# Kernel optimization log

Measured on AMD Instinct MI355X. Metric: run time of the kernel, lower is better.

Reference implementation:

```python
import jax, jax.numpy as jnp
import numpy as np

KDIM = 256
KNN = 32
VALUE_EXPAND = 4
EPS = 1e-5


def _ln_last(x, w):
    # LayerNorm over last axis with affine weight w (no bias)
    m = jnp.mean(x, axis=-1, keepdims=True)
    v = jnp.var(x, axis=-1, keepdims=True)
    return (x - m) * jax.lax.rsqrt(v + EPS) * w


def setup_inputs() -> dict:
    key = jax.random.key(0)
    ks = jax.random.split(key, 10)
    B, S, H = 2, 2048, 2048
    head, rank, mh = 2, 2, 2
    key_num = 1024
    value_num = 262144
    vvn = VALUE_EXPAND * value_num  # 1048576
    vdim = 256
    return {
        "hidden_state": jax.random.normal(ks[0], (B, S, H), jnp.float32),
        "wq": jax.random.normal(ks[1], (H, 2 * KDIM), jnp.float32) / np.sqrt(KDIM),
        "qnorm_w": jnp.full((KDIM,), 1.0 / KDIM ** 0.33, jnp.float32),
        "knorm_w": jnp.full((KDIM,), 1.0 / KDIM ** 0.33, jnp.float32),
        "keys": jax.random.normal(ks[2], (head, 2, key_num, KDIM, rank), jnp.float32) / np.sqrt(KDIM),
        "tucker_core": jax.random.uniform(ks[3], (mh, head, rank, rank), jnp.float32),
        "tucker_u": jax.random.normal(ks[4], (1, head, 1, rank), jnp.float32),
        "tucker_v": jax.random.normal(ks[5], (1, head, 1, rank), jnp.float32),
        "values": jax.random.normal(ks[6], (value_num, vdim), jnp.float32) * 0.02,
        "wv": jax.random.normal(ks[7], (VALUE_EXPAND * vdim, H), jnp.float32) / np.sqrt(VALUE_EXPAND * vdim),
        "shuffle_index": jax.random.permutation(ks[8], vvn).astype(jnp.int32),
    }


def reference(hidden_state, wq, qnorm_w, knorm_w, keys, tucker_core,
              tucker_u, tucker_v, values, wv, shuffle_index):
    B, S, H = hidden_state.shape
    bs = B * S
    head, _, key_num, kdim, rank = keys.shape
    value_num, vdim = values.shape

    # query projection + per-half layernorm
    q = (hidden_state.reshape(bs, H) @ wq).reshape(bs, 2, kdim)
    q = _ln_last(q, qnorm_w)
    q1, q2 = q[:, 0], q[:, 1]  # (bs, kdim)

    # keys layernorm over kdim (axis=-2)
    km = jnp.mean(keys, axis=-2, keepdims=True)
    kv = jnp.var(keys, axis=-2, keepdims=True)
    keysn = (keys - km) * jax.lax.rsqrt(kv + EPS) * knorm_w[:, None]

    # per-head, per-rank inner products (all heads share the single query; nhead_share_query=2)
    s1r = jnp.einsum("bd,hkdr->bhkr", q1, keysn[:, 0])  # (bs, head, key_num, rank)
    s2r = jnp.einsum("bd,hkdr->bhkr", q2, keysn[:, 1])

    # rank-1 tucker fused scores + topk along keys
    s1 = (s1r * tucker_u).sum(-1)  # (bs, head, key_num)
    s2 = (s2r * tucker_v).sum(-1)
    _, i1 = jax.lax.top_k(s1, KNN)  # (bs, head, knn)
    _, i2 = jax.lax.top_k(s2, KNN)

    g1 = jnp.take_along_axis(s1r, i1[..., None], axis=2)  # (bs, head, knn, rank)
    g2 = jnp.take_along_axis(s2r, i2[..., None], axis=2)

    # full tucker scores on the knn x knn candidate grid, summed over tucker heads
    all_scores = jnp.einsum("bhkr,mhrs,bhls->bhkl", g1, tucker_core, g2).reshape(bs, head, KNN * KNN)
    all_indices = (i1[..., :, None] * key_num + i2[..., None, :]).reshape(bs, head, KNN * KNN)

    best_scores, bi = jax.lax.top_k(all_scores, KNN)  # (bs, head, knn)
    best_indice = jnp.take_along_axis(all_indices, bi, axis=-1)

    # implicit value expansion: shuffled virtual index -> (expand slot, real value)
    shuffled = shuffle_index[best_indice]
    vidx = shuffled % value_num
    eidx = shuffled // value_num  # in [0, VALUE_EXPAND)
    vals = values[vidx]  # (bs, head, knn, vdim)
    w = jax.nn.softmax(best_scores, axis=-1)
    oh = jax.nn.one_hot(eidx, VALUE_EXPAND, dtype=vals.dtype)  # (bs, head, knn, E)
    agg = jnp.einsum("bhke,bhkv->bev", oh, w[..., None] * vals).reshape(bs, VALUE_EXPAND * vdim)
    out = agg @ wv  # (bs, H)
    return out.reshape(B, S, H)
```

## Files before the change

### kernel.cpp

```cpp
#include <hip/hip_runtime.h>
#include <float.h>
#include <math.h>


typedef __attribute__((ext_vector_type(8))) __bf16 bf16x8;
typedef __attribute__((ext_vector_type(4))) float f32x4;

__device__ __forceinline__ unsigned short f2bf(float x) {
  unsigned int u = __float_as_uint(x);
  return (unsigned short)((u + 0x7FFFu + ((u >> 16) & 1u)) >> 16);
}

__device__ __forceinline__ float wave_sum(float x) {
#pragma unroll
  for (int o = 32; o; o >>= 1) x += __shfl_xor(x, o, 64);
  return x;
}

__device__ __forceinline__ void gll16(const float* g, float* l) {
  __builtin_amdgcn_global_load_lds(
      (const __attribute__((address_space(1))) void*)g,
      (__attribute__((address_space(3))) void*)l, 16, 0, 0);
}

__device__ __forceinline__ unsigned int f2key(float f) {
  const unsigned int u = __float_as_uint(f);
  return u ^ (((unsigned int)((int)u >> 31)) | 0x80000000u);
}
__device__ __forceinline__ float key2f(unsigned int k) {
  return __uint_as_float((k & 0x80000000u) ? (k ^ 0x80000000u) : ~k);
}

__global__ void k_prep32(const float* __restrict__ keys, const float* __restrict__ knw,
                         const float* __restrict__ tu, const float* __restrict__ tv,
                         unsigned short* __restrict__ Bctbf, float* __restrict__ Bg) {
  const int bid = blockIdx.x;
  const int lane = threadIdx.x;
  const int k = bid & 1023, h = (bid >> 10) & 1, c = bid >> 11;
  const float* base = keys + (size_t)((h * 2 + c) * 1024 + k) * 512;
  float x0[4], x1[4];
  float s0 = 0.f, s1 = 0.f, sq0 = 0.f, sq1 = 0.f;
#pragma unroll
  for (int i = 0; i < 4; ++i) {
    const int d = lane + i * 64;
    const float2 p = *(const float2*)&base[d * 2];
    x0[i] = p.x; x1[i] = p.y;
    s0 += p.x; sq0 += p.x * p.x;
    s1 += p.y; sq1 += p.y * p.y;
  }
  s0 = wave_sum(s0); sq0 = wave_sum(sq0);
  s1 = wave_sum(s1); sq1 = wave_sum(sq1);
  const float m0 = s0 * (1.f / 256.f), m1 = s1 * (1.f / 256.f);
  const float rs0 = 1.f / sqrtf(sq0 * (1.f / 256.f) - m0 * m0 + 1e-5f);
  const float rs1 = 1.f / sqrtf(sq1 * (1.f / 256.f) - m1 * m1 + 1e-5f);
  const float* uv = c ? tv : tu;
  const float u0 = uv[h * 2 + 0], u1 = uv[h * 2 + 1];
  const int chk = c * 2048 + h * 1024 + k;
  float* bg = Bg + (size_t)chk * 512;
  unsigned short* bc = Bctbf + (size_t)chk * 256;
#pragma unroll
  for (int i = 0; i < 4; ++i) {
    const int d = lane + i * 64;
    const float w = knw[d];
    const float y0 = (x0[i] - m0) * rs0 * w;
    const float y1 = (x1[i] - m1) * rs1 * w;
    bg[d] = y0;
    bg[256 + d] = y1;
    bc[d] = f2bf(y0 * u0 + y1 * u1);
  }
}

__global__ __launch_bounds__(256) void k_tr32(const float* __restrict__ src,
                                              float* __restrict__ dst, int R, int C) {
  __shared__ float t[64][65];
  const int br = blockIdx.x * 64, bc = blockIdx.y * 64;
  const int tid = threadIdx.x;
  for (int idx = tid; idx < 4096; idx += 256) {
    const int r = idx >> 6, c = idx & 63;
    t[r][c] = src[(size_t)(br + r) * C + bc + c];
  }
  __syncthreads();
  for (int idx = tid; idx < 4096; idx += 256) {
    const int cc = idx >> 6, rr = idx & 63;
    dst[(size_t)(bc + cc) * R + br + rr] = t[rr][cc];
  }
}

template <int SPLITK>
__global__ __launch_bounds__(256) void k_gemm32(
    const float* __restrict__ AT, int lda,
    const float* __restrict__ BT, int ldb, int bsk, int m_split,
    float* __restrict__ C, int M, int N, int K) {
  constexpr int BK = 16;
  __shared__ float As[2][BK][128];
  __shared__ float Bs[2][BK][128];
  const int tid = threadIdx.x;
  const int lane = tid & 63;
  const int w = tid >> 6;
  const int tx = tid & 15, ty = tid >> 4;
  const int bm = blockIdx.x * 128, bn = blockIdx.y * 128;
  const int bcol = bn + ((bm >= m_split) ? bsk : 0);
  const int Ks = K / SPLITK;
  const int kbeg = blockIdx.z * Ks;
  float* Cp = C + (size_t)blockIdx.z * M * N;
  const int l5 = lane >> 5, l31 = lane & 31;
  float acc[8][8] = {};

  auto stage = [&](int buf, int t) {
    const int k0 = t * BK;
#pragma unroll
    for (int i = 0; i < 2; ++i) {
      const int rr = w * 4 + i * 2;
      const size_t krow = (size_t)(kbeg + k0 + rr + l5);
      gll16(&AT[krow * lda + bm + l31 * 4], &As[buf][rr][0]);
      gll16(&BT[krow * ldb + bcol + l31 * 4], &Bs[buf][rr][0]);
    }
  };

  const int T = Ks / BK;
  stage(0, 0);
  __syncthreads();
  int cur = 0;
  for (int t = 0; t < T; ++t) {
    if (t + 1 < T) stage(cur ^ 1, t + 1);
#pragma unroll
    for (int kk = 0; kk < BK; ++kk) {
      float a[8], b[8];
      *(float4*)&a[0] = *(const float4*)&As[cur][kk][ty * 4];
      *(float4*)&a[4] = *(const float4*)&As[cur][kk][64 + ty * 4];
      *(float4*)&b[0] = *(const float4*)&Bs[cur][kk][tx * 4];
      *(float4*)&b[4] = *(const float4*)&Bs[cur][kk][64 + tx * 4];
#pragma unroll
      for (int i = 0; i < 8; ++i)
#pragma unroll
        for (int j = 0; j < 8; ++j) acc[i][j] += a[i] * b[j];
    }
    __syncthreads();
    cur ^= 1;
  }
#pragma unroll
  for (int ih = 0; ih < 2; ++ih)
#pragma unroll
    for (int i = 0; i < 4; ++i) {
      const size_t r = bm + ih * 64 + ty * 4 + i;
#pragma unroll
      for (int jh = 0; jh < 2; ++jh) {
        float4 v = {acc[ih * 4 + i][jh * 4 + 0], acc[ih * 4 + i][jh * 4 + 1],
                    acc[ih * 4 + i][jh * 4 + 2], acc[ih * 4 + i][jh * 4 + 3]};
        *(float4*)&Cp[r * N + bn + jh * 64 + tx * 4] = v;
      }
    }
}

__global__ void k_ln_q(const float* __restrict__ qpart, const float* __restrict__ qnw,
                       float* __restrict__ q12n, unsigned short* __restrict__ q12bf) {
  const int bid = blockIdx.x;
  const int lane = threadIdx.x;
  const int b = bid >> 1, c = bid & 1;
  float x[4] = {};
#pragma unroll
  for (int s = 0; s < 4; ++s) {
    const float4 p = *(const float4*)&qpart[(size_t)s * 4096 * 512 + (size_t)b * 512 + c * 256 + lane * 4];
    x[0] += p.x; x[1] += p.y; x[2] += p.z; x[3] += p.w;
  }
  float sm = x[0] + x[1] + x[2] + x[3];
  float sq = x[0] * x[0] + x[1] * x[1] + x[2] * x[2] + x[3] * x[3];
  sm = wave_sum(sm);
  sq = wave_sum(sq);
  const float mean = sm * (1.f / 256.f);
  const float rs = 1.f / sqrtf(sq * (1.f / 256.f) - mean * mean + 1e-5f);
  const float4 w4 = *(const float4*)&qnw[lane * 4];
  float4 o;
  o.x = (x[0] - mean) * rs * w4.x;
  o.y = (x[1] - mean) * rs * w4.y;
  o.z = (x[2] - mean) * rs * w4.z;
  o.w = (x[3] - mean) * rs * w4.w;
  const size_t base = (size_t)(c * 4096 + b) * 256 + lane * 4;
  *(float4*)&q12n[base] = o;
  ushort4 ob;
  ob.x = f2bf(o.x); ob.y = f2bf(o.y); ob.z = f2bf(o.z); ob.w = f2bf(o.w);
  *(ushort4*)&q12bf[base] = ob;
}

__global__ void k_topk1(const float* __restrict__ s_r,
                        int* __restrict__ i1c, int* __restrict__ i2c) {
  const int bid = blockIdx.x;
  const int side = bid >> 13;
  const int bh = bid & 8191;
  const int b = bh >> 1, h = bh & 1;
  const int lane = threadIdx.x;
  const float* row = s_r + (size_t)(side * 4096 + b) * 2048 + h * 1024;
  unsigned int ku[16];
#pragma unroll
  for (int i = 0; i < 16; ++i) ku[i] = f2key(row[lane + (i << 6)]);
  unsigned int T = 0u;
  for (int bpos = 31; bpos >= 0; --bpos) {
    const unsigned int cand = T | (1u << bpos);
    int c = 0;
#pragma unroll
    for (int i = 0; i < 16; ++i) c += (int)__popcll(__ballot(ku[i] >= cand));
    if (c >= 48) T = cand;
  }
  int cgt = 0, ceq = 0;
#pragma unroll
  for (int i = 0; i < 16; ++i) {
    cgt += (ku[i] > T) ? 1 : 0;
    ceq += (ku[i] == T) ? 1 : 0;
  }
  int pgt = cgt, peq = ceq;
#pragma unroll
  for (int o = 1; o < 64; o <<= 1) {
    const int t1 = __shfl_up(pgt, o, 64);
    const int t2 = __shfl_up(peq, o, 64);
    if (lane >= o) { pgt += t1; peq += t2; }
  }
  const int total_gt = __shfl(pgt, 63, 64);
  const int need_eq = 48 - total_gt;
  int sgt = pgt - cgt;
  int seq = peq - ceq;
  int* iout = (side ? i2c : i1c) + bh * 48;
#pragma unroll
  for (int i = 0; i < 16; ++i) {
    const int idx = (i << 6) + lane;
    if (ku[i] > T) {
      iout[sgt++] = idx;
    } else if (ku[i] == T) {
      if (seq < need_eq) iout[total_gt + seq] = idx;
      ++seq;
    }
  }
}

__global__ __launch_bounds__(256) void k_sel(
    const float* __restrict__ q12n, const float* __restrict__ Bg,
    const int* __restrict__ i1c, const int* __restrict__ i2c,
    const float* __restrict__ tu, const float* __restrict__ tv,
    int* __restrict__ i1, int* __restrict__ i2,
    float* __restrict__ g1, float* __restrict__ g2) {
  __shared__ float qs[256];
  __shared__ int ssel[48];
  __shared__ float sc[48], sd0[48], sd1[48];
  const int bid = blockIdx.x;
  const int side = bid >> 13;
  const int bh = bid & 8191;
  const int b = bh >> 1, h = bh & 1;
  const int tid = threadIdx.x;
  if (tid < 64) {
    *(float4*)&qs[tid * 4] =
        *(const float4*)&q12n[(size_t)(side * 4096 + b) * 256 + tid * 4];
  } else if (tid < 112) {
    ssel[tid - 64] = (side ? i2c : i1c)[bh * 48 + (tid - 64)];
  }
  __syncthreads();
  const int g = tid >> 2, c4 = tid & 3;
  if (g < 48) {
    const int sel = ssel[g];
    const float* kbase = Bg + (size_t)((side * 2048 + h * 1024 + sel) * 2) * 256;
    float d0 = 0.f, d1 = 0.f;
#pragma unroll
    for (int r = 0; r < 2; ++r) {
      const float* krow = kbase + r * 256;
      float px = 0.f, py = 0.f, pz = 0.f, pw = 0.f;
#pragma unroll
      for (int i = 0; i < 16; ++i) {
        const int e = (i * 4 + c4) * 4;
        const float4 kv = *(const float4*)&krow[e];
        const float4 qv = *(const float4*)&qs[e];
        px += kv.x * qv.x;
        py += kv.y * qv.y;
        pz += kv.z * qv.z;
        pw += kv.w * qv.w;
      }
      float a = (px + py) + (pz + pw);
      a += __shfl_xor(a, 1, 64);
      a += __shfl_xor(a, 2, 64);
      if (r == 0) d0 = a; else d1 = a;
    }
    if (c4 == 0) {
      const float* uv = side ? tv : tu;
      sd0[g] = d0;
      sd1[g] = d1;
      sc[g] = d0 * uv[h * 2 + 0] + d1 * uv[h * 2 + 1];
    }
  }
  __syncthreads();
  if (tid < 64) {
    const int lane = tid;
    const unsigned int kv = (lane < 48) ? f2key(sc[lane]) : 0u;
    unsigned int T = 0u;
    for (int bpos = 31; bpos >= 0; --bpos) {
      const unsigned int cand = T | (1u << bpos);
      const int c = (int)__popcll(__ballot(kv >= cand));
      if (c >= 32) T = cand;
    }
    const unsigned long long mgt = __ballot(kv > T);
    const unsigned long long meq = __ballot((kv == T) && (lane < 48));
    const unsigned long long below = ((unsigned long long)1 << lane) - 1;
    const int total_gt = (int)__popcll(mgt);
    const int need = 32 - total_gt;
    int slot = -1;
    if (kv > T) {
      slot = (int)__popcll(mgt & below);
    } else if (kv == T && lane < 48) {
      const int r = (int)__popcll(meq & below);
      if (r < need) slot = total_gt + r;
    }
    if (slot >= 0) {
      int* iout = (side ? i2 : i1) + bh * 32;
      float* gout = (side ? g2 : g1) + (size_t)bh * 64;
      iout[slot] = ssel[lane];
      gout[slot * 2 + 0] = sd0[lane];
      gout[slot * 2 + 1] = sd1[lane];
    }
  }
}

__global__ void k_stage2(const float* __restrict__ g1, const float* __restrict__ g2,
                         const int* __restrict__ i1, const int* __restrict__ i2,
                         const float* __restrict__ tucker_core,
                         const int* __restrict__ shuffle_index,
                         float* __restrict__ w_out, int* __restrict__ sh_out) {
  __shared__ float sg1x[32], sg1y[32], sg2x[32], sg2y[32];
  __shared__ int si1[32], si2[32];
  const int bh = blockIdx.x;
  const int h = bh & 1;
  const int lane = threadIdx.x;
  if (lane < 32) {
    const float2 p1 = *(const float2*)&g1[(bh * 32 + lane) * 2];
    const float2 p2 = *(const float2*)&g2[(bh * 32 + lane) * 2];
    sg1x[lane] = p1.x;
    sg1y[lane] = p1.y;
    sg2x[lane] = p2.x;
    sg2y[lane] = p2.y;
    si1[lane] = i1[bh * 32 + lane];
    si2[lane] = i2[bh * 32 + lane];
  }
  __syncthreads();
  const float c00 = tucker_core[h * 4 + 0] + tucker_core[8 + h * 4 + 0];
  const float c01 = tucker_core[h * 4 + 1] + tucker_core[8 + h * 4 + 1];
  const float c10 = tucker_core[h * 4 + 2] + tucker_core[8 + h * 4 + 2];
  const float c11 = tucker_core[h * 4 + 3] + tucker_core[8 + h * 4 + 3];
  float sv[16];
  unsigned int ku[16];
  float m = -FLT_MAX;
#pragma unroll
  for (int i = 0; i < 16; ++i) {
    const int p = lane + (i << 6);
    const int k = p >> 5, l = p & 31;
    const float a0 = sg1x[k] * c00 + sg1y[k] * c10;
    const float a1 = sg1x[k] * c01 + sg1y[k] * c11;
    sv[i] = a0 * sg2x[l] + a1 * sg2y[l];
    ku[i] = f2key(sv[i]);
    m = fmaxf(m, sv[i]);
  }
#pragma unroll
  for (int o = 32; o; o >>= 1) m = fmaxf(m, __shfl_xor(m, o, 64));
  unsigned int T = 0u;
  for (int bpos = 31; bpos >= 0; --bpos) {
    const unsigned int cand = T | (1u << bpos);
    int c = 0;
#pragma unroll
    for (int i = 0; i < 16; ++i) c += (int)__popcll(__ballot(ku[i] >= cand));
    if (c >= 32) T = cand;
  }
  int cgt = 0, ceq = 0;
  float zp = 0.f;
#pragma unroll
  for (int i = 0; i < 16; ++i) {
    if (ku[i] > T) { ++cgt; zp += expf(sv[i] - m); }
    ceq += (ku[i] == T) ? 1 : 0;
  }
  int pgt = cgt, peq = ceq;
#pragma unroll
  for (int o = 1; o < 64; o <<= 1) {
    const int t1 = __shfl_up(pgt, o, 64);
    const int t2 = __shfl_up(peq, o, 64);
    if (lane >= o) { pgt += t1; peq += t2; }
  }
  const int total_gt = __shfl(pgt, 63, 64);
  const int need_eq = 32 - total_gt;
  const float eT = expf(key2f(T) - m);
  const float Z = wave_sum(zp) + (float)need_eq * eT;
  const float rZ = 1.f / Z;
  int sgt = pgt - cgt;
  int seq = peq - ceq;
  float* wp = w_out + bh * 32;
  int* shp = sh_out + bh * 32;
#pragma unroll
  for (int i = 0; i < 16; ++i) {
    int slot = -1;
    if (ku[i] > T) {
      slot = sgt++;
    } else if (ku[i] == T) {
      if (seq < need_eq) slot = total_gt + seq;
      ++seq;
    }
    if (slot >= 0) {
      const int p = lane + (i << 6);
      const int k = p >> 5, l = p & 31;
      const int ai = si1[k] * 1024 + si2[l];
      wp[slot] = expf(sv[i] - m) * rZ;
      shp[slot] = shuffle_index[ai];
    }
  }
}

__global__ __launch_bounds__(256) void k_agg(const float* __restrict__ w_out,
                                             const int* __restrict__ sh_out,
                                             const float* __restrict__ values,
                                             unsigned short* __restrict__ aggb) {
  __shared__ float acc[4][1024];
  const int b = blockIdx.x;
  const int tid = threadIdx.x;
  const int wave = tid >> 6, lane = tid & 63;
  for (int i = tid; i < 4096; i += 256) ((float*)acc)[i] = 0.f;
  __syncthreads();
  for (int j = wave; j < 64; j += 4) {
    const float wgt = w_out[b * 64 + j];
    const int sh = sh_out[b * 64 + j];
    const int vidx = sh & 0x3FFFF;
    const int e = sh >> 18;
    const float4 v = *(const float4*)&values[(size_t)vidx * 256 + lane * 4];
    float* dst = &acc[wave][e * 256 + lane * 4];
    dst[0] += wgt * v.x;
    dst[1] += wgt * v.y;
    dst[2] += wgt * v.z;
    dst[3] += wgt * v.w;
  }
  __syncthreads();
  for (int i = tid; i < 1024; i += 256)
    aggb[(size_t)b * 1024 + i] = f2bf(acc[0][i] + acc[1][i] + acc[2][i] + acc[3][i]);
}

__global__ __launch_bounds__(256) void k_tcvt(const float* __restrict__ src,
                                              unsigned short* __restrict__ dst,
                                              int R, int C) {
  __shared__ float tile[64][65];
  const int br = blockIdx.x * 64;
  const int bc = blockIdx.y * 64;
  const int tid = threadIdx.x;
  for (int idx = tid; idx < 4096; idx += 256) {
    const int r = idx >> 6, c = idx & 63;
    tile[r][c] = src[(size_t)(br + r) * C + bc + c];
  }
  __syncthreads();
  for (int idx = tid; idx < 4096; idx += 256) {
    const int cc = idx >> 6, rr = idx & 63;
    dst[(size_t)(bc + cc) * R + br + rr] = f2bf(tile[rr][cc]);
  }
}

template <int BM, int BN>
__global__ __launch_bounds__(256) void k_mfma(const unsigned short* __restrict__ A,
                                              const unsigned short* __restrict__ Bt,
                                              float* __restrict__ C,
                                              int M, int N, int K,
                                              int bsk, int m_split) {
  constexpr int FM = BM / 32;
  constexpr int FN = BN / 32;
  __shared__ float4 As[BM * 4];
  __shared__ float4 Bs[BN * 4];
  const int tid = threadIdx.x;
  const int lane = tid & 63;
  const int w = tid >> 6;
  const int wr = w >> 1, wc = w & 1;
  const int bm = blockIdx.x * BM, bn = blockIdx.y * BN;
  const int bcol = bn + ((bm >= m_split) ? bsk : 0);
  f32x4 acc[FM][FN];
#pragma unroll
  for (int i = 0; i < FM; ++i)
#pragma unroll
    for (int j = 0; j < FN; ++j) acc[i][j] = 0.f;

  for (int k0 = 0; k0 < K; k0 += 32) {
#pragma unroll
    for (int u = 0; u < BM * 4 / 256; ++u) {
      const int q = tid + u * 256;
      const int m = q >> 2, c = q & 3;
      As[(m >> 4) * 64 + c * 16 + (m & 15)] =
          *(const float4*)&A[(size_t)(bm + m) * K + k0 + c * 8];
    }
#pragma unroll
    for (int u = 0; u < BN * 4 / 256; ++u) {
      const int q = tid + u * 256;
      const int n = q >> 2, c = q & 3;
      Bs[(n >> 4) * 64 + c * 16 + (n & 15)] =
          *(const float4*)&Bt[(size_t)(bcol + n) * K + k0 + c * 8];
    }
    __syncthreads();
    bf16x8 af[FM], bfr[FN];
#pragma unroll
    for (int i = 0; i < FM; ++i) af[i] = *(const bf16x8*)&As[(wr * FM + i) * 64 + lane];
#pragma unroll
    for (int j = 0; j < FN; ++j) bfr[j] = *(const bf16x8*)&Bs[(wc * FN + j) * 64 + lane];
#pragma unroll
    for (int i = 0; i < FM; ++i)
#pragma unroll
      for (int j = 0; j < FN; ++j)
        acc[i][j] = __builtin_amdgcn_mfma_f32_16x16x32_bf16(af[i], bfr[j], acc[i][j], 0, 0, 0);
    __syncthreads();
  }
#pragma unroll
  for (int i = 0; i < FM; ++i) {
    const int r0 = bm + (wr * FM + i) * 16 + (lane >> 4) * 4;
#pragma unroll
    for (int j = 0; j < FN; ++j) {
      const int cc = bn + (wc * FN + j) * 16 + (lane & 15);
#pragma unroll
      for (int v = 0; v < 4; ++v) C[(size_t)(r0 + v) * N + cc] = acc[i][j][v];
    }
  }
}

extern "C" void kernel_launch(void* const* d_in, const int* in_sizes, int n_in,
                              void* d_out, int out_size, void* d_ws, size_t ws_size,
                              hipStream_t stream) {
  const float* hidden = (const float*)d_in[0];
  const float* wq     = (const float*)d_in[1];
  const float* qnw    = (const float*)d_in[2];
  const float* knw    = (const float*)d_in[3];
  const float* keys   = (const float*)d_in[4];
  const float* tcore  = (const float*)d_in[5];
  const float* tu     = (const float*)d_in[6];
  const float* tv     = (const float*)d_in[7];
  const float* values = (const float*)d_in[8];
  const float* wvm    = (const float*)d_in[9];
  const int*   shuf   = (const int*)d_in[10];
  float* out = (float*)d_out;

  char* ws = (char*)d_ws;
  size_t off = 0;
  auto alloc = [&](size_t bytes) -> void* {
    void* p = ws + off;
    off += (bytes + 255) & ~(size_t)255;
    return p;
  };
  unsigned short* Bctbf = (unsigned short*)alloc((size_t)4096 * 256 * 2);
  float* Bg    = (float*)alloc((size_t)4096 * 512 * 4);
  float* q12n  = (float*)alloc((size_t)8192 * 256 * 4);
  unsigned short* q12bf = (unsigned short*)alloc((size_t)8192 * 256 * 2);
  unsigned short* wvT  = (unsigned short*)alloc((size_t)2048 * 1024 * 2);
  unsigned short* aggb = (unsigned short*)alloc((size_t)4096 * 1024 * 2);
  int*   i1c = (int*)  alloc((size_t)8192 * 48 * 4);
  int*   i2c = (int*)  alloc((size_t)8192 * 48 * 4);
  int*   i1  = (int*)  alloc((size_t)8192 * 32 * 4);
  int*   i2  = (int*)  alloc((size_t)8192 * 32 * 4);
  float* g1  = (float*)alloc((size_t)8192 * 64 * 4);
  float* g2  = (float*)alloc((size_t)8192 * 64 * 4);
  float* wgt = (float*)alloc((size_t)8192 * 32 * 4);
  int*   sho = (int*)  alloc((size_t)8192 * 32 * 4);
  float* hiddenT = (float*)alloc((size_t)2048 * 4096 * 4);
  float* big = (float*)alloc((size_t)8192 * 2048 * 4);
  float* qpart = big;
  float* s_r   = big;
  (void)ws_size; (void)in_sizes; (void)n_in; (void)out_size;

  k_prep32<<<4096, 64, 0, stream>>>(keys, knw, tu, tv, Bctbf, Bg);
  k_tcvt<<<dim3(16, 32), 256, 0, stream>>>(wvm, wvT, 1024, 2048);
  k_tr32<<<dim3(64, 32), 256, 0, stream>>>(hidden, hiddenT, 4096, 2048);
  k_gemm32<4><<<dim3(32, 4, 4), 256, 0, stream>>>(
      hiddenT, 4096, wq, 512, 0, 1 << 30, qpart, 4096, 512, 2048);
  k_ln_q<<<8192, 64, 0, stream>>>(qpart, qnw, q12n, q12bf);
  k_mfma<128, 128><<<dim3(64, 16), 256, 0, stream>>>(
      q12bf, Bctbf, s_r, 8192, 2048, 256, 2048, 4096);
  k_topk1<<<16384, 64, 0, stream>>>(s_r, i1c, i2c);
  k_sel<<<16384, 256, 0, stream>>>(q12n, Bg, i1c, i2c, tu, tv, i1, i2, g1, g2);
  k_stage2<<<8192, 64, 0, stream>>>(g1, g2, i1, i2, tcore, shuf, wgt, sho);
  k_agg<<<4096, 256, 0, stream>>>(wgt, sho, values, aggb);
  k_mfma<128, 128><<<dim3(32, 16), 256, 0, stream>>>(
      aggb, wvT, out, 4096, 2048, 1024, 0, 1 << 30);
}
```

Baseline: 393.1 us.

## Fuse transpose into q GEMM, bf16 score matrix, merge sel and stage2

Drops the separate hidden-state transpose kernel: the q-projection GEMM now reads A row-major into registers and transposes into LDS itself. The coarse score GEMM now writes bf16 instead of fp32, so top-k candidate selection reads half the bytes and bisects only 16 bits. The per-side refinement kernel and the tucker stage-2 kernel are merged into one 512-thread block per (token, head), which removes the intermediate g1/g2/i1/i2 global round-trips and one launch. Quantising the scores to bf16 coarsens the 48-candidate prefilter and can change which candidates are kept when values tie.

Measured after the change: 429.7 us. 9.3% more time.

```diff
diff --git a/kernel.cpp b/kernel.cpp
--- a/kernel.cpp
+++ b/kernel.cpp
@@ -70,28 +70,11 @@
   }
 }
 
-__global__ __launch_bounds__(256) void k_tr32(const float* __restrict__ src,
-                                              float* __restrict__ dst, int R, int C) {
-  __shared__ float t[64][65];
-  const int br = blockIdx.x * 64, bc = blockIdx.y * 64;
-  const int tid = threadIdx.x;
-  for (int idx = tid; idx < 4096; idx += 256) {
-    const int r = idx >> 6, c = idx & 63;
-    t[r][c] = src[(size_t)(br + r) * C + bc + c];
-  }
-  __syncthreads();
-  for (int idx = tid; idx < 4096; idx += 256) {
-    const int cc = idx >> 6, rr = idx & 63;
-    dst[(size_t)(bc + cc) * R + br + rr] = t[rr][cc];
-  }
-}
-
-template <int SPLITK>
-__global__ __launch_bounds__(256) void k_gemm32(
-    const float* __restrict__ AT, int lda,
-    const float* __restrict__ BT, int ldb, int bsk, int m_split,
-    float* __restrict__ C, int M, int N, int K) {
+__global__ __launch_bounds__(256) void k_qgemm(const float* __restrict__ A,
+                                               const float* __restrict__ B,
+                                               float* __restrict__ C) {
   constexpr int BK = 16;
+  constexpr int K = 2048, N = 512;
   __shared__ float As[2][BK][128];
   __shared__ float Bs[2][BK][128];
   const int tid = threadIdx.x;
@@ -99,30 +82,53 @@
   const int w = tid >> 6;
   const int tx = tid & 15, ty = tid >> 4;
   const int bm = blockIdx.x * 128, bn = blockIdx.y * 128;
-  const int bcol = bn + ((bm >= m_split) ? bsk : 0);
-  const int Ks = K / SPLITK;
-  const int kbeg = blockIdx.z * Ks;
-  float* Cp = C + (size_t)blockIdx.z * M * N;
+  const int kbeg = blockIdx.z * 512;
+  float* Cp = C + (size_t)blockIdx.z * 4096 * 512;
   const int l5 = lane >> 5, l31 = lane & 31;
   float acc[8][8] = {};
-
-  auto stage = [&](int buf, int t) {
-    const int k0 = t * BK;
+  float4 ar[2];
+
+  auto regloadA = [&](int t) {
+    const int k0 = kbeg + t * BK;
+#pragma unroll
+    for (int u = 0; u < 2; ++u) {
+      const int q = tid + u * 256;
+      const int m = q >> 2, kc = q & 3;
+      ar[u] = *(const float4*)&A[(size_t)(bm + m) * K + k0 + kc * 4];
+    }
+  };
+  auto dswriteA = [&](int buf) {
+#pragma unroll
+    for (int u = 0; u < 2; ++u) {
+      const int q = tid + u * 256;
+      const int m = q >> 2, kc = q & 3;
+      As[buf][kc * 4 + 0][m] = ar[u].x;
+      As[buf][kc * 4 + 1][m] = ar[u].y;
+      As[buf][kc * 4 + 2][m] = ar[u].z;
+      As[buf][kc * 4 + 3][m] = ar[u].w;
+    }
+  };
+  auto stageB = [&](int buf, int t) {
+    const int k0 = kbeg + t * BK;
 #pragma unroll
     for (int i = 0; i < 2; ++i) {
       const int rr = w * 4 + i * 2;
-      const size_t krow = (size_t)(kbeg + k0 + rr + l5);
-      gll16(&AT[krow * lda + bm + l31 * 4], &As[buf][rr][0]);
-      gll16(&BT[krow * ldb + bcol + l31 * 4], &Bs[buf][rr][0]);
+      const size_t krow = (size_t)(k0 + rr + l5);
+      gll16(&B[krow * N + bn + l31 * 4], &Bs[buf][rr][0]);
     }
   };
 
-  const int T = Ks / BK;
-  stage(0, 0);
+  regloadA(0);
+  stageB(0, 0);
+  dswriteA(0);
   __syncthreads();
   int cur = 0;
+  const int T = 512 / BK;
   for (int t = 0; t < T; ++t) {
-    if (t + 1 < T) stage(cur ^ 1, t + 1);
+    if (t + 1 < T) {
+      regloadA(t + 1);
+      stageB(cur ^ 1, t + 1);
+    }
 #pragma unroll
     for (int kk = 0; kk < BK; ++kk) {
       float a[8], b[8];
@@ -135,6 +141,7 @@
 #pragma unroll
         for (int j = 0; j < 8; ++j) acc[i][j] += a[i] * b[j];
     }
+    if (t + 1 < T) dswriteA(cur ^ 1);
     __syncthreads();
     cur ^= 1;
   }
@@ -182,19 +189,29 @@
   *(ushort4*)&q12bf[base] = ob;
 }
 
-__global__ void k_topk1(const float* __restrict__ s_r,
+__global__ void k_topk1(const unsigned short* __restrict__ s_r,
                         int* __restrict__ i1c, int* __restrict__ i2c) {
   const int bid = blockIdx.x;
   const int side = bid >> 13;
   const int bh = bid & 8191;
   const int b = bh >> 1, h = bh & 1;
   const int lane = threadIdx.x;
-  const float* row = s_r + (size_t)(side * 4096 + b) * 2048 + h * 1024;
+  const unsigned short* row = s_r + (size_t)(side * 4096 + b) * 2048 + h * 1024;
   unsigned int ku[16];
-#pragma unroll
-  for (int i = 0; i < 16; ++i) ku[i] = f2key(row[lane + (i << 6)]);
+  {
+    const uint4 a = *(const uint4*)&row[lane * 16];
+    const uint4 bq = *(const uint4*)&row[lane * 16 + 8];
+    const unsigned int words[8] = {a.x, a.y, a.z, a.w, bq.x, bq.y, bq.z, bq.w};
+#pragma unroll
+    for (int j = 0; j < 8; ++j) {
+      const unsigned int lo = words[j] & 0xFFFFu;
+      const unsigned int hi = words[j] >> 16;
+      ku[2 * j] = lo ^ ((lo & 0x8000u) ? 0xFFFFu : 0x8000u);
+      ku[2 * j + 1] = hi ^ ((hi & 0x8000u) ? 0xFFFFu : 0x8000u);
+    }
+  }
   unsigned int T = 0u;
-  for (int bpos = 31; bpos >= 0; --bpos) {
+  for (int bpos = 15; bpos >= 0; --bpos) {
     const unsigned int cand = T | (1u << bpos);
     int c = 0;
 #pragma unroll
@@ -221,7 +238,7 @@
   int* iout = (side ? i2c : i1c) + bh * 48;
 #pragma unroll
   for (int i = 0; i < 16; ++i) {
-    const int idx = (i << 6) + lane;
+    const int idx = lane * 16 + i;
     if (ku[i] > T) {
       iout[sgt++] = idx;
     } else if (ku[i] == T) {
@@ -231,31 +248,39 @@
   }
 }
 
-__global__ __launch_bounds__(256) void k_sel(
+__global__ __launch_bounds__(512) void k_sel2(
     const float* __restrict__ q12n, const float* __restrict__ Bg,
     const int* __restrict__ i1c, const int* __restrict__ i2c,
     const float* __restrict__ tu, const float* __restrict__ tv,
-    int* __restrict__ i1, int* __restrict__ i2,
-    float* __restrict__ g1, float* __restrict__ g2) {
-  __shared__ float qs[256];
-  __shared__ int ssel[48];
-  __shared__ float sc[48], sd0[48], sd1[48];
-  const int bid = blockIdx.x;
-  const int side = bid >> 13;
-  const int bh = bid & 8191;
+    const float* __restrict__ tucker_core, const int* __restrict__ shuffle_index,
+    float* __restrict__ w_out, int* __restrict__ sh_out) {
+  __shared__ float qs[2][256];
+  __shared__ int ssel[2][48];
+  __shared__ float sc[2][48], sd0s[2][48], sd1s[2][48];
+  __shared__ float sgx[2][32], sgy[2][32];
+  __shared__ int si32[2][32];
+  const int bh = blockIdx.x;
   const int b = bh >> 1, h = bh & 1;
   const int tid = threadIdx.x;
-  if (tid < 64) {
-    *(float4*)&qs[tid * 4] =
-        *(const float4*)&q12n[(size_t)(side * 4096 + b) * 256 + tid * 4];
-  } else if (tid < 112) {
-    ssel[tid - 64] = (side ? i2c : i1c)[bh * 48 + (tid - 64)];
-  }
-  __syncthreads();
-  const int g = tid >> 2, c4 = tid & 3;
+  if (tid < 128) {
+    const int sd = tid >> 6, t = tid & 63;
+    *(float4*)&qs[sd][t * 4] =
+        *(const float4*)&q12n[(size_t)(sd * 4096 + b) * 256 + t * 4];
+  } else if (tid < 224) {
+    const int j = tid - 128;
+    const int sd = (j >= 48) ? 1 : 0;
+    const int jj = j - sd * 48;
+    ssel[sd][jj] = (sd ? i2c : i1c)[bh * 48 + jj];
+  }
+  __syncthreads();
+  const int w = tid >> 6;
+  const int sd = (w >= 4) ? 1 : 0;
+  const int local = tid - sd * 256;
+  const int g = local >> 2, c4 = local & 3;
   if (g < 48) {
-    const int sel = ssel[g];
-    const float* kbase = Bg + (size_t)((side * 2048 + h * 1024 + sel) * 2) * 256;
+    const int sel = ssel[sd][g];
+    const float* kbase = Bg + (size_t)((sd * 2048 + h * 1024 + sel) * 2) * 256;
+    const float* qp = qs[sd];
     float d0 = 0.f, d1 = 0.f;
 #pragma unroll
     for (int r = 0; r < 2; ++r) {
@@ -265,7 +290,7 @@
       for (int i = 0; i < 16; ++i) {
         const int e = (i * 4 + c4) * 4;
         const float4 kv = *(const float4*)&krow[e];
-        const float4 qv = *(const float4*)&qs[e];
+        const float4 qv = *(const float4*)&qp[e];
         px += kv.x * qv.x;
         py += kv.y * qv.y;
         pz += kv.z * qv.z;
@@ -277,21 +302,21 @@
       if (r == 0) d0 = a; else d1 = a;
     }
     if (c4 == 0) {
-      const float* uv = side ? tv : tu;
-      sd0[g] = d0;
-      sd1[g] = d1;
-      sc[g] = d0 * uv[h * 2 + 0] + d1 * uv[h * 2 + 1];
-    }
-  }
-  __syncthreads();
-  if (tid < 64) {
-    const int lane = tid;
-    const unsigned int kv = (lane < 48) ? f2key(sc[lane]) : 0u;
+      const float* uv = sd ? tv : tu;
+      sd0s[sd][g] = d0;
+      sd1s[sd][g] = d1;
+      sc[sd][g] = d0 * uv[h * 2 + 0] + d1 * uv[h * 2 + 1];
+    }
+  }
+  __syncthreads();
+  if (w == 0 || w == 4) {
+    const int s2 = (w == 4) ? 1 : 0;
+    const int lane = tid & 63;
+    const unsigned int kv = (lane < 48) ? f2key(sc[s2][lane]) : 0u;
     unsigned int T = 0u;
     for (int bpos = 31; bpos >= 0; --bpos) {
       const unsigned int cand = T | (1u << bpos);
-      const int c = (int)__popcll(__ballot(kv >= cand));
-      if (c >= 32) T = cand;
+      if ((int)__popcll(__ballot(kv >= cand)) >= 32) T = cand;
     }
     const unsigned long long mgt = __ballot(kv > T);
     const unsigned long long meq = __ballot((kv == T) && (lane < 48));
@@ -306,101 +331,80 @@
       if (r < need) slot = total_gt + r;
     }
     if (slot >= 0) {
-      int* iout = (side ? i2 : i1) + bh * 32;
-      float* gout = (side ? g2 : g1) + (size_t)bh * 64;
-      iout[slot] = ssel[lane];
-      gout[slot * 2 + 0] = sd0[lane];
-      gout[slot * 2 + 1] = sd1[lane];
-    }
-  }
-}
-
-__global__ void k_stage2(const float* __restrict__ g1, const float* __restrict__ g2,
-                         const int* __restrict__ i1, const int* __restrict__ i2,
-                         const float* __restrict__ tucker_core,
-                         const int* __restrict__ shuffle_index,
-                         float* __restrict__ w_out, int* __restrict__ sh_out) {
-  __shared__ float sg1x[32], sg1y[32], sg2x[32], sg2y[32];
-  __shared__ int si1[32], si2[32];
-  const int bh = blockIdx.x;
-  const int h = bh & 1;
-  const int lane = threadIdx.x;
-  if (lane < 32) {
-    const float2 p1 = *(const float2*)&g1[(bh * 32 + lane) * 2];
-    const float2 p2 = *(const float2*)&g2[(bh * 32 + lane) * 2];
-    sg1x[lane] = p1.x;
-    sg1y[lane] = p1.y;
-    sg2x[lane] = p2.x;
-    sg2y[lane] = p2.y;
-    si1[lane] = i1[bh * 32 + lane];
-    si2[lane] = i2[bh * 32 + lane];
-  }
-  __syncthreads();
-  const float c00 = tucker_core[h * 4 + 0] + tucker_core[8 + h * 4 + 0];
-  const float c01 = tucker_core[h * 4 + 1] + tucker_core[8 + h * 4 + 1];
-  const float c10 = tucker_core[h * 4 + 2] + tucker_core[8 + h * 4 + 2];
-  const float c11 = tucker_core[h * 4 + 3] + tucker_core[8 + h * 4 + 3];
-  float sv[16];
-  unsigned int ku[16];
-  float m = -FLT_MAX;
-#pragma unroll
-  for (int i = 0; i < 16; ++i) {
-    const int p = lane + (i << 6);
-    const int k = p >> 5, l = p & 31;
-    const float a0 = sg1x[k] * c00 + sg1y[k] * c10;
-    const float a1 = sg1x[k] * c01 + sg1y[k] * c11;
-    sv[i] = a0 * sg2x[l] + a1 * sg2y[l];
-    ku[i] = f2key(sv[i]);
-    m = fmaxf(m, sv[i]);
-  }
-#pragma unroll
-  for (int o = 32; o; o >>= 1) m = fmaxf(m, __shfl_xor(m, o, 64));
-  unsigned int T = 0u;
-  for (int bpos = 31; bpos >= 0; --bpos) {
-    const unsigned int cand = T | (1u << bpos);
-    int c = 0;
-#pragma unroll
-    for (int i = 0; i < 16; ++i) c += (int)__popcll(__ballot(ku[i] >= cand));
-    if (c >= 32) T = cand;
-  }
-  int cgt = 0, ceq = 0;
-  float zp = 0.f;
-#pragma unroll
-  for (int i = 0; i < 16; ++i) {
-    if (ku[i] > T) { ++cgt; zp += expf(sv[i] - m); }
-    ceq += (ku[i] == T) ? 1 : 0;
-  }
-  int pgt = cgt, peq = ceq;
-#pragma unroll
-  for (int o = 1; o < 64; o <<= 1) {
-    const int t1 = __shfl_up(pgt, o, 64);
-    const int t2 = __shfl_up(peq, o, 64);
-    if (lane >= o) { pgt += t1; peq += t2; }
-  }
-  const int total_gt = __shfl(pgt, 63, 64);
-  const int need_eq = 32 - total_gt;
-  const float eT = expf(key2f(T) - m);
-  const float Z = wave_sum(zp) + (float)need_eq * eT;
-  const float rZ = 1.f / Z;
-  int sgt = pgt - cgt;
-  int seq = peq - ceq;
-  float* wp = w_out + bh * 32;
-  int* shp = sh_out + bh * 32;
-#pragma unroll
-  for (int i = 0; i < 16; ++i) {
-    int slot = -1;
-    if (ku[i] > T) {
-      slot = sgt++;
-    } else if (ku[i] == T) {
-      if (seq < need_eq) slot = total_gt + seq;
-      ++seq;
-    }
-    if (slot >= 0) {
+      si32[s2][slot] = ssel[s2][lane];
+      sgx[s2][slot] = sd0s[s2][lane];
+      sgy[s2][slot] = sd1s[s2][lane];
+    }
+  }
+  __syncthreads();
+  if (w == 0) {
+    const int lane = tid;
+    const float c00 = tucker_core[h * 4 + 0] + tucker_core[8 + h * 4 + 0];
+    const float c01 = tucker_core[h * 4 + 1] + tucker_core[8 + h * 4 + 1];
+    const float c10 = tucker_core[h * 4 + 2] + tucker_core[8 + h * 4 + 2];
+    const float c11 = tucker_core[h * 4 + 3] + tucker_core[8 + h * 4 + 3];
+    float sv[16];
+    unsigned int ku[16];
+    float m = -FLT_MAX;
+#pragma unroll
+    for (int i = 0; i < 16; ++i) {
       const int p = lane + (i << 6);
       const int k = p >> 5, l = p & 31;
-      const int ai = si1[k] * 1024 + si2[l];
-      wp[slot] = expf(sv[i] - m) * rZ;
-      shp[slot] = shuffle_index[ai];
+      const float a0 = sgx[0][k] * c00 + sgy[0][k] * c10;
+      const float a1 = sgx[0][k] * c01 + sgy[0][k] * c11;
+      sv[i] = a0 * sgx[1][l] + a1 * sgy[1][l];
+      ku[i] = f2key(sv[i]);
+      m = fmaxf(m, sv[i]);
+    }
+#pragma unroll
+    for (int o = 32; o; o >>= 1) m = fmaxf(m, __shfl_xor(m, o, 64));
+    unsigned int T = 0u;
+    for (int bpos = 31; bpos >= 0; --bpos) {
+      const unsigned int cand = T | (1u << bpos);
+      int c = 0;
+#pragma unroll
+      for (int i = 0; i < 16; ++i) c += (int)__popcll(__ballot(ku[i] >= cand));
+      if (c >= 32) T = cand;
+    }
+    int cgt = 0, ceq = 0;
+    float zp = 0.f;
+#pragma unroll
+    for (int i = 0; i < 16; ++i) {
+      if (ku[i] > T) { ++cgt; zp += expf(sv[i] - m); }
+      ceq += (ku[i] == T) ? 1 : 0;
+    }
+    int pgt = cgt, peq = ceq;
+#pragma unroll
+    for (int o = 1; o < 64; o <<= 1) {
+      const int t1 = __shfl_up(pgt, o, 64);
+      const int t2 = __shfl_up(peq, o, 64);
+      if (lane >= o) { pgt += t1; peq += t2; }
+    }
+    const int total_gt = __shfl(pgt, 63, 64);
+    const int need_eq = 32 - total_gt;
+    const float eT = expf(key2f(T) - m);
+    const float Z = wave_sum(zp) + (float)need_eq * eT;
+    const float rZ = 1.f / Z;
+    int sgt = pgt - cgt;
+    int seq = peq - ceq;
+    float* wp = w_out + bh * 32;
+    int* shp = sh_out + bh * 32;
+#pragma unroll
+    for (int i = 0; i < 16; ++i) {
+      int slot = -1;
+      if (ku[i] > T) {
+        slot = sgt++;
+      } else if (ku[i] == T) {
+        if (seq < need_eq) slot = total_gt + seq;
+        ++seq;
+      }
+      if (slot >= 0) {
+        const int p = lane + (i << 6);
+        const int k = p >> 5, l = p & 31;
+        const int ai = si32[0][k] * 1024 + si32[1][l];
+        wp[slot] = expf(sv[i] - m) * rZ;
+        shp[slot] = shuffle_index[ai];
+      }
     }
   }
 }
@@ -450,10 +454,10 @@
   }
 }
 
-template <int BM, int BN>
+template <int BM, int BN, bool OBF>
 __global__ __launch_bounds__(256) void k_mfma(const unsigned short* __restrict__ A,
                                               const unsigned short* __restrict__ Bt,
-                                              float* __restrict__ C,
+                                              void* __restrict__ Cv,
                                               int M, int N, int K,
                                               int bsk, int m_split) {
   constexpr int FM = BM / 32;
@@ -507,7 +511,12 @@
     for (int j = 0; j < FN; ++j) {
       const int cc = bn + (wc * FN + j) * 16 + (lane & 15);
 #pragma unroll
-      for (int v = 0; v < 4; ++v) C[(size_t)(r0 + v) * N + cc] = acc[i][j][v];
+      for (int v = 0; v < 4; ++v) {
+        if (OBF)
+          ((unsigned short*)Cv)[(size_t)(r0 + v) * N + cc] = f2bf(acc[i][j][v]);
+        else
+          ((float*)Cv)[(size_t)(r0 + v) * N + cc] = acc[i][j][v];
+      }
     }
   }
 }
@@ -543,30 +552,23 @@
   unsigned short* aggb = (unsigned short*)alloc((size_t)4096 * 1024 * 2);
   int*   i1c = (int*)  alloc((size_t)8192 * 48 * 4);
   int*   i2c = (int*)  alloc((size_t)8192 * 48 * 4);
-  int*   i1  = (int*)  alloc((size_t)8192 * 32 * 4);
-  int*   i2  = (int*)  alloc((size_t)8192 * 32 * 4);
-  float* g1  = (float*)alloc((size_t)8192 * 64 * 4);
-  float* g2  = (float*)alloc((size_t)8192 * 64 * 4);
   float* wgt = (float*)alloc((size_t)8192 * 32 * 4);
   int*   sho = (int*)  alloc((size_t)8192 * 32 * 4);
-  float* hiddenT = (float*)alloc((size_t)2048 * 4096 * 4);
   float* big = (float*)alloc((size_t)8192 * 2048 * 4);
   float* qpart = big;
-  float* s_r   = big;
+  unsigned short* s_r = (unsigned short*)big;
   (void)ws_size; (void)in_sizes; (void)n_in; (void)out_size;
 
   k_prep32<<<4096, 64, 0, stream>>>(keys, knw, tu, tv, Bctbf, Bg);
   k_tcvt<<<dim3(16, 32), 256, 0, stream>>>(wvm, wvT, 1024, 2048);
-  k_tr32<<<dim3(64, 32), 256, 0, stream>>>(hidden, hiddenT, 4096, 2048);
-  k_gemm32<4><<<dim3(32, 4, 4), 256, 0, stream>>>(
-      hiddenT, 4096, wq, 512, 0, 1 << 30, qpart, 4096, 512, 2048);
+  k_qgemm<<<dim3(32, 4, 4), 256, 0, stream>>>(hidden, wq, qpart);
   k_ln_q<<<8192, 64, 0, stream>>>(qpart, qnw, q12n, q12bf);
-  k_mfma<128, 128><<<dim3(64, 16), 256, 0, stream>>>(
+  k_mfma<128, 128, true><<<dim3(64, 16), 256, 0, stream>>>(
       q12bf, Bctbf, s_r, 8192, 2048, 256, 2048, 4096);
   k_topk1<<<16384, 64, 0, stream>>>(s_r, i1c, i2c);
-  k_sel<<<16384, 256, 0, stream>>>(q12n, Bg, i1c, i2c, tu, tv, i1, i2, g1, g2);
-  k_stage2<<<8192, 64, 0, stream>>>(g1, g2, i1, i2, tcore, shuf, wgt, sho);
+  k_sel2<<<8192, 512, 0, stream>>>(q12n, Bg, i1c, i2c, tu, tv, tcore, shuf,
+                                   wgt, sho);
   k_agg<<<4096, 256, 0, stream>>>(wgt, sho, values, aggb);
-  k_mfma<128, 128><<<dim3(32, 16), 256, 0, stream>>>(
+  k_mfma<128, 128, false><<<dim3(32, 16), 256, 0, stream>>>(
       aggb, wvT, out, 4096, 2048, 1024, 0, 1 << 30);
 }
```
